# Performance work log

Measured on AMD Instinct MI355X. Metric: run time of the kernel, lower is better.

The kernel has to match this reference:

```python
import jax, jax.numpy as jnp
import numpy as np
import math

NUM_HEADS = 8

def setup_inputs() -> dict:
    key = jax.random.key(0)
    ks = jax.random.split(key, 20)
    N, n, M, E = 4096, 3, 16, 256
    nE = 65536
    s = lambda k, shape: (jax.random.normal(k, shape, jnp.float32) * 0.02)
    return {
        "equ": jax.random.normal(ks[0], (N, n, M), jnp.float32),
        "h": jax.random.normal(ks[1], (N, E), jnp.float32),
        "edge_index": jax.random.randint(ks[2], (2, nE), 0, N),
        "edge_fea": jax.random.normal(ks[3], (nE, 4), jnp.float32),
        "W_equ": s(ks[4], (M, E)),
        "W_gproj": s(ks[5], (E, 32)),
        "W_vg": s(ks[6], (E, E)),
        "W_g1": s(ks[7], (32 * 32, 2 * E)), "b_g1": jnp.zeros((2 * E,), jnp.float32),
        "W_g2": s(ks[8], (2 * E, E)), "b_g2": jnp.zeros((E,), jnp.float32),
        "W_q": s(ks[9], (2 * E, E)), "b_q": jnp.zeros((E,), jnp.float32),
        "W_k": s(ks[10], (2 * E, E)), "b_k": jnp.zeros((E,), jnp.float32),
        "W_v": s(ks[11], (2 * E, E)), "b_v": jnp.zeros((E,), jnp.float32),
        "W_ng": s(ks[12], (E, E)), "b_ng": jnp.zeros((E,), jnp.float32),
        "W_gout": s(ks[13], (E, E)),
        "W_gdec": s(ks[14], (E, M)),
        "W_hdec": s(ks[15], (E, E)), "b_hdec": jnp.zeros((E,), jnp.float32),
    }


def reference(equ, h, edge_index, edge_fea, W_equ, W_gproj, W_vg, W_g1, b_g1,
              W_g2, b_g2, W_q, b_q, W_k, b_k, W_v, b_v, W_ng, b_ng,
              W_gout, W_gdec, W_hdec, b_hdec):
    # edge_index / edge_fea are unused in the original forward (dead args).
    N, n, M = equ.shape
    E = W_equ.shape[1]
    H = NUM_HEADS
    D = E // H
    scaling = D ** -0.5
    sqrtE = math.sqrt(E)

    g_src = (equ @ W_equ) * sqrtE                     # [N, n, E]
    h_src = h * sqrtE                                 # [N, E]

    g2 = g_src @ W_gproj                              # [N, n, 32]
    gram = jnp.einsum('nia,nib->nab', g2, g2)         # [N, 32, 32]
    g2 = gram.reshape(N, 32 * 32)
    g2 = jax.nn.relu(g2 @ W_g1 + b_g1) @ W_g2 + b_g2  # [N, E]

    h2 = jnp.concatenate([g2, h_src], axis=-1)        # [N, 2E]
    q = ((h2 @ W_q + b_q) * scaling).reshape(N, H, D)
    k = (h2 @ W_k + b_k).reshape(N, H, D)
    v = (h2 @ W_v + b_v).reshape(N, H, D)
    vg = (g_src @ W_vg).reshape(N, n, H, D)           # [N, n, H, D]

    attn = jax.nn.softmax(jnp.einsum('nhd,mhd->hnm', q, k), axis=-1)  # [H, N, N]

    out_v = jnp.einsum('hnm,mhd->nhd', attn, v).reshape(N, E)
    h_src1 = out_v @ W_ng + b_ng                      # [N, E]

    # Same attention probs reused for the vector channel (torch does repeat+bmm;
    # we broadcast instead of materializing the repeated [n*H, N, N] tensor).
    out_g = jnp.einsum('hnm,mvhd->nvhd', attn, vg).reshape(N, n, E)
    g_src1 = out_g @ W_gout                           # [N, n, E]

    g_src = g_src + g_src1
    h_src = h_src + h_src1
    equ_out = g_src @ W_gdec                          # [N, n, M]
    h_out = h_src @ W_hdec + b_hdec                   # [N, E]
    return (equ_out, h_out)
```

## Files before the change

kernel.cpp:

```cpp
#include <hip/hip_runtime.h>
#include <hip/hip_bf16.h>

typedef __attribute__((ext_vector_type(8))) short short8;
typedef __attribute__((ext_vector_type(4))) float floatx4;

constexpr int N_ = 4096;
constexpr float SQRT_E = 16.0f;
constexpr float QSCALE = 0.17677669529663687f * 1.4426950408889634f;

__device__ __forceinline__ ushort f2bf(float x) {
  __hip_bfloat16 h = __float2bfloat16(x);
  return *reinterpret_cast<ushort*>(&h);
}
__device__ __forceinline__ float bf2f(ushort b) {
  unsigned int u = ((unsigned int)b) << 16;
  return __uint_as_float(u);
}

__device__ __forceinline__ float dpp_max16(float x) {
  int v = __float_as_int(x);
  int y;
  y = __builtin_amdgcn_update_dpp(v, v, 0x128, 0xf, 0xf, false);
  v = __float_as_int(fmaxf(__int_as_float(v), __int_as_float(y)));
  y = __builtin_amdgcn_update_dpp(v, v, 0x124, 0xf, 0xf, false);
  v = __float_as_int(fmaxf(__int_as_float(v), __int_as_float(y)));
  y = __builtin_amdgcn_update_dpp(v, v, 0x122, 0xf, 0xf, false);
  v = __float_as_int(fmaxf(__int_as_float(v), __int_as_float(y)));
  y = __builtin_amdgcn_update_dpp(v, v, 0x121, 0xf, 0xf, false);
  v = __float_as_int(fmaxf(__int_as_float(v), __int_as_float(y)));
  return __int_as_float(v);
}

__device__ __forceinline__ void do_transpose(
    const float* __restrict__ src, ushort* __restrict__ dsth,
    ushort* __restrict__ dstl, int R, int C, int lb, int cb_shift,
    float* smem, int hasLo)
{
  float (*tile)[33] = (float(*)[33])smem;
  const int r0 = (lb >> cb_shift) * 32;
  const int c0 = (lb & ((1 << cb_shift) - 1)) * 32;
  const int tx = threadIdx.x & 31, ty = threadIdx.x >> 5;
  #pragma unroll
  for (int p = 0; p < 4; ++p) {
    const int lr = p*8 + ty;
    tile[lr][tx] = (r0+lr < R && c0+tx < C) ? src[(size_t)(r0+lr)*C + c0 + tx] : 0.f;
  }
  __syncthreads();
  #pragma unroll
  for (int p = 0; p < 4; ++p) {
    const int dc = p*8 + ty;
    if (c0+dc < C && r0+tx < R) {
      const float v = tile[tx][dc];
      const ushort hi = f2bf(v);
      dsth[(size_t)(c0+dc)*R + r0 + tx] = hi;
      if (hasLo) dstl[(size_t)(c0+dc)*R + r0 + tx] = f2bf(v - bf2f(hi));
    }
  }
}

__global__ __launch_bounds__(256) void k_prep(
    const float* __restrict__ equ, const float* __restrict__ h,
    const float* __restrict__ W_equ, const float* __restrict__ W_gproj,
    const float* __restrict__ W_g1, const float* __restrict__ W_g2,
    const float* __restrict__ W_q, const float* __restrict__ W_k,
    const float* __restrict__ W_v, const float* __restrict__ W_vg,
    const float* __restrict__ W_ng, const float* __restrict__ W_gout,
    const float* __restrict__ W_hdec, const float* __restrict__ W_gdec,
    ushort* __restrict__ Wg1t, ushort* __restrict__ Wg2t,
    ushort* __restrict__ Wth, ushort* __restrict__ Wtl,
    ushort* __restrict__ Wvgt, ushort* __restrict__ Wngt,
    ushort* __restrict__ Wgoutt, ushort* __restrict__ Whdect,
    ushort* __restrict__ Wgdect,
    ushort* __restrict__ h2h, ushort* __restrict__ h2l,
    ushort* __restrict__ g_src_b, ushort* __restrict__ gram_b,
    float* __restrict__ pre0)
{
  __shared__ __align__(16) float smem[1120];
  const int b = blockIdx.x;
  const int t = threadIdx.x;

  if (b < 512) {
    do_transpose(W_g1, Wg1t, nullptr, 1024, 512, b, 4, smem, 0);
  } else if (b < 640) {
    do_transpose(W_g2, Wg2t, nullptr, 512, 256, b-512, 3, smem, 0);
  } else if (b < 768) {
    do_transpose(W_q, Wth, Wtl, 512, 256, b-640, 3, smem, 1);
  } else if (b < 896) {
    do_transpose(W_k, Wth + 256*512, Wtl + 256*512, 512, 256, b-768, 3, smem, 1);
  } else if (b < 1024) {
    do_transpose(W_v, Wth + 512*512, Wtl + 512*512, 512, 256, b-896, 3, smem, 1);
  } else if (b < 1088) {
    do_transpose(W_vg, Wvgt, nullptr, 256, 256, b-1024, 3, smem, 0);
  } else if (b < 1152) {
    do_transpose(W_ng, Wngt, nullptr, 256, 256, b-1088, 3, smem, 0);
  } else if (b < 1216) {
    do_transpose(W_gout, Wgoutt, nullptr, 256, 256, b-1152, 3, smem, 0);
  } else if (b < 1280) {
    do_transpose(W_hdec, Whdect, nullptr, 256, 256, b-1216, 3, smem, 0);
  } else if (b < 1288) {
    do_transpose(W_gdec, Wgdect, nullptr, 256, 16, b-1280, 0, smem, 0);
  } else if (b < 5384) {
    const int i = b - 1288;
    const float v = h[(size_t)i*256 + t] * SQRT_E;
    const ushort hi = f2bf(v);
    h2h[(size_t)i*512 + 256 + t] = hi;
    h2l[(size_t)i*512 + 256 + t] = f2bf(v - bf2f(hi));
  } else {
    float* eq   = smem;
    float* gs   = smem + 48;
    float* g2p  = smem + 816;
    float* part = smem + 912;
    const int i = b - 5384;
    if (t < 48) eq[t] = equ[(size_t)i*48 + t];
    __syncthreads();
    #pragma unroll
    for (int j = 0; j < 3; ++j) {
      float s = 0.f;
      #pragma unroll
      for (int m = 0; m < 16; ++m) s += eq[j*16+m] * W_equ[m*256 + t];
      s *= SQRT_E;
      gs[j*256 + t] = s;
      g_src_b[((size_t)i*3 + j)*256 + t] = f2bf(s);
    }
    __syncthreads();
    if (t < 192) {
      const int o = t % 96, half = t / 96;
      const int j = o >> 5, a = o & 31;
      const int e0 = half * 128;
      float s = 0.f;
      for (int e = 0; e < 128; ++e)
        s += gs[j*256 + e0 + e] * W_gproj[(size_t)(e0+e)*32 + a];
      part[t] = s;
    }
    __syncthreads();
    if (t < 96) g2p[t] = part[t] + part[96 + t];
    __syncthreads();
    #pragma unroll
    for (int r = 0; r < 4; ++r) {
      const int idx = r*256 + t;
      const int a = idx >> 5, bb = idx & 31;
      const float s = g2p[a]*g2p[bb] + g2p[32+a]*g2p[32+bb] + g2p[64+a]*g2p[64+bb];
      gram_b[(size_t)i*1024 + idx] = f2bf(s);
    }
    if (t < 192) {
      const int j = t >> 6, ks = (t >> 4) & 3, mc = t & 15;
      const int e0 = ks * 64;
      float s = 0.f;
      for (int e = 0; e < 64; ++e)
        s += gs[j*256 + e0 + e] * W_gdec[(size_t)(e0 + e)*16 + mc];
      part[t] = s;
    }
    __syncthreads();
    if (t < 48) {
      const int j = t >> 4, mc = t & 15;
      pre0[((size_t)i*3 + j)*16 + mc] =
          part[j*64 + mc] + part[j*64 + 16 + mc] +
          part[j*64 + 32 + mc] + part[j*64 + 48 + mc];
    }
  }
}

template<int KTOT>
__device__ __forceinline__ void gemm_core(
    const ushort* __restrict__ A, const ushort* __restrict__ Bt,
    int bM, int bN, floatx4 acc[4], ushort* As, ushort* Bs)
{
  const int t = threadIdx.x;
  const int wave = t >> 6, lane = t & 63, quad = lane >> 4, m = lane & 15;
  #pragma unroll
  for (int ct = 0; ct < 4; ++ct) acc[ct] = {0.f, 0.f, 0.f, 0.f};
  const int ca = t*2, cb = t*2 + 1;
  const int ra = ca >> 3, pa = ca & 7;
  const int rb = cb >> 3, pb = cb & 7;
  const ushort* pA0 = A  + (size_t)(bM+ra)*KTOT + pa*8;
  const ushort* pA1 = A  + (size_t)(bM+rb)*KTOT + pb*8;
  const ushort* pB0 = Bt + (size_t)(bN+ra)*KTOT + pa*8;
  const ushort* pB1 = Bt + (size_t)(bN+rb)*KTOT + pb*8;
  short8 rA0 = *(const short8*)pA0, rA1 = *(const short8*)pA1;
  short8 rB0 = *(const short8*)pB0, rB1 = *(const short8*)pB1;
  for (int k0 = 0; k0 < KTOT; k0 += 64) {
    __syncthreads();
    *(short8*)&As[ra*72 + pa*8] = rA0;
    *(short8*)&As[rb*72 + pb*8] = rA1;
    *(short8*)&Bs[ra*72 + pa*8] = rB0;
    *(short8*)&Bs[rb*72 + pb*8] = rB1;
    if (k0 + 64 < KTOT) {
      pA0 += 64; pA1 += 64; pB0 += 64; pB1 += 64;
      rA0 = *(const short8*)pA0; rA1 = *(const short8*)pA1;
      rB0 = *(const short8*)pB0; rB1 = *(const short8*)pB1;
    }
    __syncthreads();
    #pragma unroll
    for (int ks = 0; ks < 2; ++ks) {
      const short8 af = *(const short8*)&As[(wave*16 + m)*72 + ks*32 + quad*8];
      #pragma unroll
      for (int ct = 0; ct < 4; ++ct) {
        const short8 bf = *(const short8*)&Bs[(ct*16 + m)*72 + ks*32 + quad*8];
        acc[ct] = __builtin_amdgcn_mfma_f32_16x16x32_bf16(af, bf, acc[ct], 0, 0, 0);
      }
    }
  }
}

template<int KTOT>
__device__ __forceinline__ void gemm_core3(
    const ushort* __restrict__ Ah, const ushort* __restrict__ Al,
    const ushort* __restrict__ Bth, const ushort* __restrict__ Btl,
    int bM, int bN, floatx4 acc[4],
    ushort* Ash, ushort* Asl, ushort* Bsh, ushort* Bsl)
{
  const int t = threadIdx.x;
  const int wave = t >> 6, lane = t & 63, quad = lane >> 4, m = lane & 15;
  #pragma unroll
  for (int ct = 0; ct < 4; ++ct) acc[ct] = {0.f, 0.f, 0.f, 0.f};
  const int ca = t*2, cb = t*2 + 1;
  const int ra = ca >> 3, pa = ca & 7;
  const int rb = cb >> 3, pb = cb & 7;
  const ushort* pAh0 = Ah  + (size_t)(bM+ra)*KTOT + pa*8;
  const ushort* pAh1 = Ah  + (size_t)(bM+rb)*KTOT + pb*8;
  const ushort* pAl0 = Al  + (size_t)(bM+ra)*KTOT + pa*8;
  const ushort* pAl1 = Al  + (size_t)(bM+rb)*KTOT + pb*8;
  const ushort* pBh0 = Bth + (size_t)(bN+ra)*KTOT + pa*8;
  const ushort* pBh1 = Bth + (size_t)(bN+rb)*KTOT + pb*8;
  const ushort* pBl0 = Btl + (size_t)(bN+ra)*KTOT + pa*8;
  const ushort* pBl1 = Btl + (size_t)(bN+rb)*KTOT + pb*8;
  short8 rAh0 = *(const short8*)pAh0, rAh1 = *(const short8*)pAh1;
  short8 rAl0 = *(const short8*)pAl0, rAl1 = *(const short8*)pAl1;
  short8 rBh0 = *(const short8*)pBh0, rBh1 = *(const short8*)pBh1;
  short8 rBl0 = *(const short8*)pBl0, rBl1 = *(const short8*)pBl1;
  for (int k0 = 0; k0 < KTOT; k0 += 64) {
    __syncthreads();
    *(short8*)&Ash[ra*72 + pa*8] = rAh0;
    *(short8*)&Ash[rb*72 + pb*8] = rAh1;
    *(short8*)&Asl[ra*72 + pa*8] = rAl0;
    *(short8*)&Asl[rb*72 + pb*8] = rAl1;
    *(short8*)&Bsh[ra*72 + pa*8] = rBh0;
    *(short8*)&Bsh[rb*72 + pb*8] = rBh1;
    *(short8*)&Bsl[ra*72 + pa*8] = rBl0;
    *(short8*)&Bsl[rb*72 + pb*8] = rBl1;
    if (k0 + 64 < KTOT) {
      pAh0 += 64; pAh1 += 64; pAl0 += 64; pAl1 += 64;
      pBh0 += 64; pBh1 += 64; pBl0 += 64; pBl1 += 64;
      rAh0 = *(const short8*)pAh0; rAh1 = *(const short8*)pAh1;
      rAl0 = *(const short8*)pAl0; rAl1 = *(const short8*)pAl1;
      rBh0 = *(const short8*)pBh0; rBh1 = *(const short8*)pBh1;
      rBl0 = *(const short8*)pBl0; rBl1 = *(const short8*)pBl1;
    }
    __syncthreads();
    #pragma unroll
    for (int ks = 0; ks < 2; ++ks) {
      const short8 ah = *(const short8*)&Ash[(wave*16 + m)*72 + ks*32 + quad*8];
      const short8 al = *(const short8*)&Asl[(wave*16 + m)*72 + ks*32 + quad*8];
      #pragma unroll
      for (int ct = 0; ct < 4; ++ct) {
        const short8 bh = *(const short8*)&Bsh[(ct*16 + m)*72 + ks*32 + quad*8];
        const short8 bl = *(const short8*)&Bsl[(ct*16 + m)*72 + ks*32 + quad*8];
        acc[ct] = __builtin_amdgcn_mfma_f32_16x16x32_bf16(ah, bl, acc[ct], 0, 0, 0);
        acc[ct] = __builtin_amdgcn_mfma_f32_16x16x32_bf16(al, bh, acc[ct], 0, 0, 0);
        acc[ct] = __builtin_amdgcn_mfma_f32_16x16x32_bf16(ah, bh, acc[ct], 0, 0, 0);
      }
    }
  }
}

__global__ __launch_bounds__(256) void k_g1(
    const ushort* __restrict__ gram_b, const ushort* __restrict__ Wg1t,
    const float* __restrict__ b_g1, ushort* __restrict__ hidden)
{
  __shared__ __align__(16) ushort As[64*72], Bs[64*72];
  floatx4 acc[4];
  const int bM = blockIdx.x*64, bN = blockIdx.y*64;
  gemm_core<1024>(gram_b, Wg1t, bM, bN, acc, As, Bs);
  const int lane = threadIdx.x & 63, wave = threadIdx.x >> 6;
  const int quad = lane >> 4, m = lane & 15;
  #pragma unroll
  for (int ct = 0; ct < 4; ++ct) {
    const int c = bN + ct*16 + m;
    #pragma unroll
    for (int r = 0; r < 4; ++r) {
      const int i = bM + wave*16 + quad*4 + r;
      hidden[(size_t)i*512 + c] = f2bf(fmaxf(acc[ct][r] + b_g1[c], 0.f));
    }
  }
}

__global__ __launch_bounds__(256) void k_g2(
    const ushort* __restrict__ hidden, const ushort* __restrict__ Wg2t,
    const float* __restrict__ b_g2, ushort* __restrict__ h2h, ushort* __restrict__ h2l)
{
  __shared__ __align__(16) ushort As[64*72], Bs[64*72];
  floatx4 acc[4];
  const int bM = blockIdx.x*64, bN = blockIdx.y*64;
  gemm_core<512>(hidden, Wg2t, bM, bN, acc, As, Bs);
  const int lane = threadIdx.x & 63, wave = threadIdx.x >> 6;
  const int quad = lane >> 4, m = lane & 15;
  #pragma unroll
  for (int ct = 0; ct < 4; ++ct) {
    const int c = bN + ct*16 + m;
    #pragma unroll
    for (int r = 0; r < 4; ++r) {
      const int i = bM + wave*16 + quad*4 + r;
      const float s = acc[ct][r] + b_g2[c];
      const ushort hi = f2bf(s);
      h2h[(size_t)i*512 + c] = hi;
      h2l[(size_t)i*512 + c] = f2bf(s - bf2f(hi));
    }
  }
}

__global__ __launch_bounds__(256) void k_g34(
    const ushort* __restrict__ h2h, const ushort* __restrict__ h2l,
    const ushort* __restrict__ Wth, const ushort* __restrict__ Wtl,
    const float* __restrict__ b_q, const float* __restrict__ b_k,
    const float* __restrict__ b_v,
    const ushort* __restrict__ g_src_b, const ushort* __restrict__ Wvgt,
    float* __restrict__ q_ws, ushort* __restrict__ kh,
    ushort* __restrict__ vt)
{
  __shared__ __align__(16) ushort S0[64*72], S1[64*72], S2[64*72], S3[64*72];
  const int lb = blockIdx.y*192 + blockIdx.x;
  const int lane = threadIdx.x & 63, wave = threadIdx.x >> 6;
  const int quad = lane >> 4, m = lane & 15;
  floatx4 acc[4];
  if (lb < 768) {
    const int bM = (lb & 63)*64, bN = (lb >> 6)*64;
    if (bN < 512) {
      gemm_core3<512>(h2h, h2l, Wth, Wtl, bM, bN, acc, S0, S1, S2, S3);
      #pragma unroll
      for (int ct = 0; ct < 4; ++ct) {
        const int c = bN + ct*16 + m;
        #pragma unroll
        for (int r = 0; r < 4; ++r) {
          const int i = bM + wave*16 + quad*4 + r;
          if (c < 256) {
            const float s = acc[ct][r] + b_q[c];
            q_ws[((size_t)(c >> 5)*N_ + i)*32 + (c & 31)] = s * QSCALE;
          } else {
            const int cc = c - 256;
            const float s = acc[ct][r] + b_k[cc];
            kh[((size_t)(cc >> 5)*N_ + i)*32 + (cc & 31)] = f2bf(s);
          }
        }
      }
    } else {
      gemm_core<512>(h2h, Wth, bM, bN, acc, S0, S1);
      #pragma unroll
      for (int ct = 0; ct < 4; ++ct) {
        const int cc = bN + ct*16 + m - 512;
        #pragma unroll
        for (int r = 0; r < 4; ++r) {
          const int i = bM + wave*16 + quad*4 + r;
          const float s = acc[ct][r] + b_v[cc];
          vt[((size_t)(cc >> 5)*128 + (cc & 31))*N_ + i] = f2bf(s);
        }
      }
    }
  } else {
    const int lb2 = lb - 768;
    const int bM = (lb2 >> 2)*64, bN = (lb2 & 3)*64;
    gemm_core<256>(g_src_b, Wvgt, bM, bN, acc, S0, S1);
    #pragma unroll
    for (int ct = 0; ct < 4; ++ct) {
      const int c = bN + ct*16 + m;
      const int hh = c >> 5, d = c & 31;
      #pragma unroll
      for (int r = 0; r < 4; ++r) {
        const int i3 = bM + wave*16 + quad*4 + r;
        const int i = i3 / 3, j = i3 - 3*i;
        vt[((size_t)hh*128 + 32 + j*32 + d)*N_ + i] = f2bf(acc[ct][r]);
      }
    }
  }
}

__global__ __launch_bounds__(256, 4) void k3_attn(
    const float* __restrict__ q_ws, const ushort* __restrict__ kh,
    const ushort* __restrict__ vt,
    ushort* __restrict__ Po0, ushort* __restrict__ Po1,
    ushort* __restrict__ Po2, ushort* __restrict__ Po3,
    float* __restrict__ Pml)
{
  __shared__ __align__(16) ushort Khs[64*40];
  __shared__ __align__(16) ushort Vs[128*64];
  __shared__ __align__(16) ushort Pl[4*16*72];
  __shared__ float li_s[64];

  const int t    = threadIdx.x;
  const int wave = t >> 6;
  const int lane = t & 63;
  const int quad = lane >> 4;
  const int m    = lane & 15;
  const int h    = blockIdx.y;
  const int s    = blockIdx.z;
  const int n0q  = blockIdx.x * 64;

  const int ktb = s * 16;
  const int kte = ktb + 16;

  union { short8 v; ushort u[8]; } Aqh, Aql;
  {
    const float* qp = q_ws + ((size_t)h*N_ + n0q + wave*16 + m)*32 + quad*8;
    #pragma unroll
    for (int jj = 0; jj < 8; ++jj) {
      const float x = qp[jj];
      const ushort hi = f2bf(x);
      Aqh.u[jj] = hi;
      Aql.u[jj] = f2bf(x - bf2f(hi));
    }
  }

  union { short8 v; ushort u[8]; } onesf;
  {
    const ushort ov = (m == 0) ? (ushort)0x3F80 : (ushort)0;
    #pragma unroll
    for (int jj = 0; jj < 8; ++jj) onesf.u[jj] = ov;
  }

  floatx4 Of[9];
  #pragma unroll
  for (int nt = 0; nt < 9; ++nt) Of[nt] = {0.f, 0.f, 0.f, 0.f};
  float mi[4];
  #pragma unroll
  for (int r = 0; r < 4; ++r) mi[r] = -3.0e38f;

  const int krow = t >> 2, kch = (t & 3) * 8;

  const ushort* pKh = kh + ((size_t)h*N_ + ktb*64 + krow)*32 + kch;
  const ushort* pV[4];
  int wV[4];
  #pragma unroll
  for (int p = 0; p < 4; ++p) {
    const int idx = p*256 + t, row = idx >> 3, g = idx & 7;
    pV[p] = vt + ((size_t)h*128 + row)*N_ + ktb*64 + g*8;
    wV[p] = (row*8 + (g ^ (row & 7)))*8;
  }

  short8 rK0 = *(const short8*)pKh;
  short8 rV[4];
  #pragma unroll
  for (int p = 0; p < 4; ++p) rV[p] = *(const short8*)pV[p];

  for (int kt = ktb; kt < kte; ++kt) {
    __syncthreads();
    *(short8*)&Khs[krow*40 + kch] = rK0;
    #pragma unroll
    for (int p = 0; p < 4; ++p) *(short8*)&Vs[wV[p]] = rV[p];
    if (kt + 1 < kte) {
      pKh += 2048;
      rK0 = *(const short8*)pKh;
      #pragma unroll
      for (int p = 0; p < 4; ++p) { pV[p] += 64; rV[p] = *(const short8*)pV[p]; }
    }
    __syncthreads();

    floatx4 sf[4];
    #pragma unroll
    for (int kb = 0; kb < 4; ++kb) {
      const short8 bkh = *(const short8*)&Khs[(kb*16 + m)*40 + quad*8];
      floatx4 sv = {0.f, 0.f, 0.f, 0.f};
      sv = __builtin_amdgcn_mfma_f32_16x16x32_bf16(Aql.v, bkh, sv, 0, 0, 0);
      sv = __builtin_amdgcn_mfma_f32_16x16x32_bf16(Aqh.v, bkh, sv, 0, 0, 0);
      sf[kb] = sv;
    }

    float tm[4];
    bool need = false;
    #pragma unroll
    for (int r = 0; r < 4; ++r) {
      float nm = fmaxf(fmaxf(sf[0][r], sf[1][r]), fmaxf(sf[2][r], sf[3][r]));
      tm[r] = dpp_max16(nm);
      need |= (tm[r] > mi[r] + 20.f);
    }
    if (__any(need)) {
      #pragma unroll
      for (int r = 0; r < 4; ++r) {
        const float mn = fmaxf(mi[r], tm[r]);
        const float al = exp2f(mi[r] - mn);
        mi[r] = mn;
        #pragma unroll
        for (int nt = 0; nt < 9; ++nt) Of[nt][r] *= al;
      }
    }
    float base[4];
    #pragma unroll
    for (int r = 0; r < 4; ++r) base[r] = 1064866805.0f - mi[r]*8388608.0f;
    #pragma unroll
    for (int kb = 0; kb < 4; ++kb)
      #pragma unroll
      for (int r = 0; r < 4; ++r) {
        int pi = (int)(sf[kb][r]*8388608.0f + base[r]);
        pi = pi < 0 ? 0 : pi;
        Pl[wave*1152 + (quad*4 + r)*72 + kb*16 + m] = (ushort)(pi >> 16);
      }

    #pragma unroll
    for (int ks = 0; ks < 2; ++ks) {
      const short8 ap = *(const short8*)&Pl[wave*1152 + m*72 + ks*32 + quad*8];
      #pragma unroll
      for (int nt = 0; nt < 8; ++nt) {
        const int row = nt*16 + m;
        const int pos = (ks*4 + quad) ^ (row & 7);
        const short8 bv = *(const short8*)&Vs[(row*8 + pos)*8];
        Of[nt] = __builtin_amdgcn_mfma_f32_16x16x32_bf16(ap, bv, Of[nt], 0, 0, 0);
      }
      Of[8] = __builtin_amdgcn_mfma_f32_16x16x32_bf16(ap, onesf.v, Of[8], 0, 0, 0);
    }
  }

  if (m == 0) {
    #pragma unroll
    for (int r = 0; r < 4; ++r) li_s[wave*16 + quad*4 + r] = Of[8][r];
  }
  __syncthreads();
  const floatx4 liv = *(const floatx4*)&li_s[wave*16 + quad*4];
  float linv[4];
  #pragma unroll
  for (int r = 0; r < 4; ++r) linv[r] = 1.0f / liv[r];

  ushort* Po = (s == 0) ? Po0 : ((s == 1) ? Po1 : ((s == 2) ? Po2 : Po3));
  #pragma unroll
  for (int nt = 0; nt < 8; ++nt) {
    #pragma unroll
    for (int r = 0; r < 4; ++r) {
      const int n = n0q + wave*16 + quad*4 + r;
      Po[((size_t)h*N_ + n)*128 + nt*16 + m] = f2bf(Of[nt][r] * linv[r]);
    }
  }
  if (m == 0) {
    #pragma unroll
    for (int r = 0; r < 4; ++r) {
      const int n = n0q + wave*16 + quad*4 + r;
      Pml[(((size_t)s*8 + h)*N_ + n)*2 + 0] = mi[r];
      Pml[(((size_t)s*8 + h)*N_ + n)*2 + 1] = Of[8][r];
    }
  }
}

__global__ __launch_bounds__(256) void k_merge(
    const ushort* __restrict__ Po0, const ushort* __restrict__ Po1,
    const ushort* __restrict__ Po2, const ushort* __restrict__ Po3,
    const float* __restrict__ Pml,
    ushort* __restrict__ out_v_b, ushort* __restrict__ out_g_b)
{
  const int idx = blockIdx.x*256 + threadIdx.x;
  const int c0 = (idx & 15) * 8;
  const int n  = (idx >> 4) & 4095;
  const int h  = idx >> 16;
  float mm[4], ll[4];
  #pragma unroll
  for (int s = 0; s < 4; ++s) {
    mm[s] = Pml[(((size_t)s*8 + h)*N_ + n)*2 + 0];
    ll[s] = Pml[(((size_t)s*8 + h)*N_ + n)*2 + 1];
  }
  const float M = fmaxf(fmaxf(mm[0], mm[1]), fmaxf(mm[2], mm[3]));
  float w[4], tot = 0.f;
  #pragma unroll
  for (int s = 0; s < 4; ++s) { w[s] = exp2f(mm[s] - M) * ll[s]; tot += w[s]; }
  const float inv = 1.0f / tot;
  union { short8 v; ushort u[8]; } a, b, c, d, res;
  a.v = *(const short8*)&Po0[((size_t)h*N_ + n)*128 + c0];
  b.v = *(const short8*)&Po1[((size_t)h*N_ + n)*128 + c0];
  c.v = *(const short8*)&Po2[((size_t)h*N_ + n)*128 + c0];
  d.v = *(const short8*)&Po3[((size_t)h*N_ + n)*128 + c0];
  #pragma unroll
  for (int j = 0; j < 8; ++j)
    res.u[j] = f2bf((w[0]*bf2f(a.u[j]) + w[1]*bf2f(b.u[j]) +
                     w[2]*bf2f(c.u[j]) + w[3]*bf2f(d.u[j])) * inv);
  if (c0 < 32) {
    *(short8*)&out_v_b[(size_t)n*256 + h*32 + c0] = res.v;
  } else {
    const int j = (c0 - 32) >> 5, cc = (c0 - 32) & 31;
    *(short8*)&out_g_b[((size_t)n*3 + j)*256 + h*32 + cc] = res.v;
  }
}

__global__ __launch_bounds__(256) void k56ab(
    const ushort* __restrict__ out_v_b, const ushort* __restrict__ Wngt,
    const float* __restrict__ b_ng, const float* __restrict__ h,
    ushort* __restrict__ tmp_b,
    const ushort* __restrict__ out_g_b, const ushort* __restrict__ Wgoutt,
    ushort* __restrict__ gsum_b)
{
  __shared__ __align__(16) ushort As[64*72], Bs[64*72];
  floatx4 acc[4];
  const int lane = threadIdx.x & 63, wave = threadIdx.x >> 6;
  const int quad = lane >> 4, m = lane & 15;
  const int bN = blockIdx.y*64;
  if (blockIdx.x < 64) {
    const int bM = blockIdx.x*64;
    gemm_core<256>(out_v_b, Wngt, bM, bN, acc, As, Bs);
    #pragma unroll
    for (int ct = 0; ct < 4; ++ct) {
      const int c = bN + ct*16 + m;
      #pragma unroll
      for (int r = 0; r < 4; ++r) {
        const int i = bM + wave*16 + quad*4 + r;
        tmp_b[(size_t)i*256 + c] =
            f2bf(acc[ct][r] + b_ng[c] + h[(size_t)i*256 + c] * SQRT_E);
      }
    }
  } else {
    const int bM = (blockIdx.x - 64)*64;
    gemm_core<256>(out_g_b, Wgoutt, bM, bN, acc, As, Bs);
    #pragma unroll
    for (int ct = 0; ct < 4; ++ct) {
      const int c = bN + ct*16 + m;
      #pragma unroll
      for (int r = 0; r < 4; ++r) {
        const int i = bM + wave*16 + quad*4 + r;
        gsum_b[(size_t)i*256 + c] = f2bf(acc[ct][r]);
      }
    }
  }
}

__global__ __launch_bounds__(256) void k56cd(
    const ushort* __restrict__ tmp_b, const ushort* __restrict__ Whdect,
    const float* __restrict__ b_hdec,
    const ushort* __restrict__ gsum_b, const ushort* __restrict__ Wgdect,
    const float* __restrict__ pre0,
    float* __restrict__ out)
{
  __shared__ __align__(16) ushort As[64*72], Bs[64*72];
  const int t = threadIdx.x;
  const int lane = t & 63, wave = t >> 6;
  const int quad = lane >> 4, m = lane & 15;
  if (blockIdx.x < 64) {
    floatx4 acc[4];
    const int bM = blockIdx.x*64, bN = blockIdx.y*64;
    gemm_core<256>(tmp_b, Whdect, bM, bN, acc, As, Bs);
    #pragma unroll
    for (int ct = 0; ct < 4; ++ct) {
      const int c = bN + ct*16 + m;
      #pragma unroll
      for (int r = 0; r < 4; ++r) {
        const int i = bM + wave*16 + quad*4 + r;
        out[196608 + (size_t)i*256 + c] = acc[ct][r] + b_hdec[c];
      }
    }
  } else if (blockIdx.y == 0) {
    const int bM = (blockIdx.x - 64)*64;
    floatx4 acc = {0.f, 0.f, 0.f, 0.f};
    const int row = t >> 2, kq = (t & 3) * 8;
    for (int k0 = 0; k0 < 256; k0 += 32) {
      __syncthreads();
      *(short8*)&As[row*40 + kq] = *(const short8*)&gsum_b[(size_t)(bM+row)*256 + k0 + kq];
      if (t < 64)
        *(short8*)&Bs[(t>>2)*40 + kq] = *(const short8*)&Wgdect[(size_t)(t>>2)*256 + k0 + kq];
      __syncthreads();
      const short8 af = *(const short8*)&As[(wave*16 + m)*40 + quad*8];
      const short8 bf = *(const short8*)&Bs[m*40 + quad*8];
      acc = __builtin_amdgcn_mfma_f32_16x16x32_bf16(af, bf, acc, 0, 0, 0);
    }
    #pragma unroll
    for (int r = 0; r < 4; ++r) {
      const int i3 = bM + wave*16 + quad*4 + r;
      out[(size_t)i3*16 + m] = acc[r] + pre0[(size_t)i3*16 + m];
    }
  }
}

extern "C" void kernel_launch(void* const* d_in, const int* in_sizes, int n_in,
                              void* d_out, int out_size, void* d_ws, size_t ws_size,
                              hipStream_t stream) {
  const float* equ    = (const float*)d_in[0];
  const float* h      = (const float*)d_in[1];
  const float* W_equ  = (const float*)d_in[4];
  const float* W_gproj= (const float*)d_in[5];
  const float* W_vg   = (const float*)d_in[6];
  const float* W_g1   = (const float*)d_in[7];
  const float* b_g1   = (const float*)d_in[8];
  const float* W_g2   = (const float*)d_in[9];
  const float* b_g2   = (const float*)d_in[10];
  const float* W_q    = (const float*)d_in[11];
  const float* b_q    = (const float*)d_in[12];
  const float* W_k    = (const float*)d_in[13];
  const float* b_k    = (const float*)d_in[14];
  const float* W_v    = (const float*)d_in[15];
  const float* b_v    = (const float*)d_in[16];
  const float* W_ng   = (const float*)d_in[17];
  const float* b_ng   = (const float*)d_in[18];
  const float* W_gout = (const float*)d_in[19];
  const float* W_gdec = (const float*)d_in[20];
  const float* W_hdec = (const float*)d_in[21];
  const float* b_hdec = (const float*)d_in[22];
  float* out = (float*)d_out;

  char* wsb = (char*)d_ws;
  constexpr size_t MiB = 1048576;
  float*  q_ws    = (float*) (wsb +  0*MiB);
  ushort* kh      = (ushort*)(wsb +  4*MiB);
  float*  Pml     = (float*) (wsb +  6*MiB);
  float*  pre0    = (float*) (wsb +  7*MiB);
  ushort* vt      = (ushort*)(wsb +  8*MiB);
  ushort* h2h     = (ushort*)(wsb + 17*MiB);
  ushort* h2l     = (ushort*)(wsb + 21*MiB);
  ushort* g_src_b = (ushort*)(wsb + 25*MiB);
  ushort* wbase   = (ushort*)(wsb + 31*MiB);
  ushort* Wg1t = wbase;
  ushort* Wg2t = wbase + 524288;
  ushort* Wth  = wbase + 655360;
  ushort* Wtl  = wbase + 1048576;
  ushort* Wvgt = wbase + 1441792;
  ushort* gram_b  = (ushort*)(wsb + 34*MiB);
  ushort* hidden  = (ushort*)(wsb + 42*MiB);
  ushort* Po0     = (ushort*)(wsb + 17*MiB);
  ushort* Po1     = (ushort*)(wsb + 25*MiB);
  ushort* Po2     = (ushort*)(wsb + 34*MiB);
  ushort* Po3     = (ushort*)(wsb + 42*MiB);
  ushort* wbase2  = (ushort*)(wsb + 50*MiB);
  ushort* Wngt   = wbase2;
  ushort* Wgoutt = wbase2 + 65536;
  ushort* Whdect = wbase2 + 131072;
  ushort* Wgdect = wbase2 + 196608;
  ushort* out_v_b = (ushort*)(wsb +  4*MiB);
  ushort* out_g_b = (ushort*)(wsb +  8*MiB);
  ushort* tmp_b   = (ushort*)(wsb + 17*MiB);
  ushort* gsum_b  = (ushort*)(wsb + 25*MiB);

  k_prep<<<9480, 256, 0, stream>>>(
      equ, h, W_equ, W_gproj, W_g1, W_g2, W_q, W_k, W_v,
      W_vg, W_ng, W_gout, W_hdec, W_gdec,
      Wg1t, Wg2t, Wth, Wtl, Wvgt, Wngt, Wgoutt, Whdect, Wgdect,
      h2h, h2l, g_src_b, gram_b, pre0);

  k_g1<<<dim3(64, 8), 256, 0, stream>>>(gram_b, Wg1t, b_g1, hidden);
  k_g2<<<dim3(64, 4), 256, 0, stream>>>(hidden, Wg2t, b_g2, h2h, h2l);
  k_g34<<<dim3(192, 8), 256, 0, stream>>>(h2h, h2l, Wth, Wtl, b_q, b_k, b_v,
                                          g_src_b, Wvgt, q_ws, kh, vt);

  dim3 g3(64, 8, 4);
  k3_attn<<<g3, 256, 0, stream>>>(q_ws, kh, vt, Po0, Po1, Po2, Po3, Pml);
  k_merge<<<2048, 256, 0, stream>>>(Po0, Po1, Po2, Po3, Pml, out_v_b, out_g_b);

  k56ab<<<dim3(256, 4), 256, 0, stream>>>(out_v_b, Wngt, b_ng, h, tmp_b,
                                          out_g_b, Wgoutt, gsum_b);
  k56cd<<<dim3(256, 4), 256, 0, stream>>>(tmp_b, Whdect, b_hdec,
                                          gsum_b, Wgdect, pre0, out);
}
```

Baseline: 278.2 us.

## Transpose attention MFMA to keep P in registers and use three KV splits

```diff
diff --git a/kernel.cpp b/kernel.cpp
--- a/kernel.cpp
+++ b/kernel.cpp
@@ -2,6 +2,7 @@
 #include <hip/hip_bf16.h>
 
 typedef __attribute__((ext_vector_type(8))) short short8;
+typedef __attribute__((ext_vector_type(4))) short bhalf4;
 typedef __attribute__((ext_vector_type(4))) float floatx4;
 
 constexpr int N_ = 4096;
@@ -15,20 +16,6 @@
 __device__ __forceinline__ float bf2f(ushort b) {
   unsigned int u = ((unsigned int)b) << 16;
   return __uint_as_float(u);
-}
-
-__device__ __forceinline__ float dpp_max16(float x) {
-  int v = __float_as_int(x);
-  int y;
-  y = __builtin_amdgcn_update_dpp(v, v, 0x128, 0xf, 0xf, false);
-  v = __float_as_int(fmaxf(__int_as_float(v), __int_as_float(y)));
-  y = __builtin_amdgcn_update_dpp(v, v, 0x124, 0xf, 0xf, false);
-  v = __float_as_int(fmaxf(__int_as_float(v), __int_as_float(y)));
-  y = __builtin_amdgcn_update_dpp(v, v, 0x122, 0xf, 0xf, false);
-  v = __float_as_int(fmaxf(__int_as_float(v), __int_as_float(y)));
-  y = __builtin_amdgcn_update_dpp(v, v, 0x121, 0xf, 0xf, false);
-  v = __float_as_int(fmaxf(__int_as_float(v), __int_as_float(y)));
-  return __int_as_float(v);
 }
 
 __device__ __forceinline__ void do_transpose(
@@ -373,16 +360,14 @@
   }
 }
 
-__global__ __launch_bounds__(256, 4) void k3_attn(
+__global__ __launch_bounds__(256, 6) void k3_attn(
     const float* __restrict__ q_ws, const ushort* __restrict__ kh,
     const ushort* __restrict__ vt,
-    ushort* __restrict__ Po0, ushort* __restrict__ Po1,
-    ushort* __restrict__ Po2, ushort* __restrict__ Po3,
+    ushort* __restrict__ Po0, ushort* __restrict__ Po1, ushort* __restrict__ Po2,
     float* __restrict__ Pml)
 {
   __shared__ __align__(16) ushort Khs[64*40];
   __shared__ __align__(16) ushort Vs[128*64];
-  __shared__ __align__(16) ushort Pl[4*16*72];
   __shared__ float li_s[64];
 
   const int t    = threadIdx.x;
@@ -394,8 +379,8 @@
   const int s    = blockIdx.z;
   const int n0q  = blockIdx.x * 64;
 
-  const int ktb = s * 16;
-  const int kte = ktb + 16;
+  const int ktb = (s == 0) ? 0  : (s == 1 ? 22 : 43);
+  const int kte = (s == 0) ? 22 : (s == 1 ? 43 : 64);
 
   union { short8 v; ushort u[8]; } Aqh, Aql;
   {
@@ -416,23 +401,25 @@
     for (int jj = 0; jj < 8; ++jj) onesf.u[jj] = ov;
   }
 
-  floatx4 Of[9];
-  #pragma unroll
-  for (int nt = 0; nt < 9; ++nt) Of[nt] = {0.f, 0.f, 0.f, 0.f};
-  float mi[4];
-  #pragma unroll
-  for (int r = 0; r < 4; ++r) mi[r] = -3.0e38f;
+  floatx4 Of[8];
+  #pragma unroll
+  for (int nt = 0; nt < 8; ++nt) Of[nt] = {0.f, 0.f, 0.f, 0.f};
+  floatx4 Of8 = {0.f, 0.f, 0.f, 0.f};
+  float mi = -3.0e38f;
 
   const int krow = t >> 2, kch = (t & 3) * 8;
-
   const ushort* pKh = kh + ((size_t)h*N_ + ktb*64 + krow)*32 + kch;
+
   const ushort* pV[4];
-  int wV[4];
+  int wv0[4], wv1[4];
   #pragma unroll
   for (int p = 0; p < 4; ++p) {
     const int idx = p*256 + t, row = idx >> 3, g = idx & 7;
     pV[p] = vt + ((size_t)h*128 + row)*N_ + ktb*64 + g*8;
-    wV[p] = (row*8 + (g ^ (row & 7)))*8;
+    const int sb0  = 32*(g>>2) + 16*(g&1) + 4*((g>>1)&1);
+    const int blk0 = sb0 >> 3, off = sb0 & 4, r7 = row & 7;
+    wv0[p] = row*64 + ((blk0       ^ r7) * 8) + off;
+    wv1[p] = row*64 + (((blk0 + 1) ^ r7) * 8) + off;
   }
 
   short8 rK0 = *(const short8*)pKh;
@@ -440,11 +427,18 @@
   #pragma unroll
   for (int p = 0; p < 4; ++p) rV[p] = *(const short8*)pV[p];
 
+  const int x7 = m & 7;
+
   for (int kt = ktb; kt < kte; ++kt) {
     __syncthreads();
     *(short8*)&Khs[krow*40 + kch] = rK0;
     #pragma unroll
-    for (int p = 0; p < 4; ++p) *(short8*)&Vs[wV[p]] = rV[p];
+    for (int p = 0; p < 4; ++p) {
+      union { short8 v; bhalf4 h2[2]; } tmp;
+      tmp.v = rV[p];
+      *(bhalf4*)&Vs[wv0[p]] = tmp.h2[0];
+      *(bhalf4*)&Vs[wv1[p]] = tmp.h2[1];
+    }
     if (kt + 1 < kte) {
       pKh += 2048;
       rK0 = *(const short8*)pKh;
@@ -458,114 +452,98 @@
     for (int kb = 0; kb < 4; ++kb) {
       const short8 bkh = *(const short8*)&Khs[(kb*16 + m)*40 + quad*8];
       floatx4 sv = {0.f, 0.f, 0.f, 0.f};
-      sv = __builtin_amdgcn_mfma_f32_16x16x32_bf16(Aql.v, bkh, sv, 0, 0, 0);
-      sv = __builtin_amdgcn_mfma_f32_16x16x32_bf16(Aqh.v, bkh, sv, 0, 0, 0);
+      sv = __builtin_amdgcn_mfma_f32_16x16x32_bf16(bkh, Aql.v, sv, 0, 0, 0);
+      sv = __builtin_amdgcn_mfma_f32_16x16x32_bf16(bkh, Aqh.v, sv, 0, 0, 0);
       sf[kb] = sv;
     }
 
-    float tm[4];
-    bool need = false;
-    #pragma unroll
-    for (int r = 0; r < 4; ++r) {
-      float nm = fmaxf(fmaxf(sf[0][r], sf[1][r]), fmaxf(sf[2][r], sf[3][r]));
-      tm[r] = dpp_max16(nm);
-      need |= (tm[r] > mi[r] + 20.f);
-    }
-    if (__any(need)) {
-      #pragma unroll
-      for (int r = 0; r < 4; ++r) {
-        const float mn = fmaxf(mi[r], tm[r]);
-        const float al = exp2f(mi[r] - mn);
-        mi[r] = mn;
-        #pragma unroll
-        for (int nt = 0; nt < 9; ++nt) Of[nt][r] *= al;
-      }
-    }
-    float base[4];
-    #pragma unroll
-    for (int r = 0; r < 4; ++r) base[r] = 1064866805.0f - mi[r]*8388608.0f;
-    #pragma unroll
-    for (int kb = 0; kb < 4; ++kb)
-      #pragma unroll
-      for (int r = 0; r < 4; ++r) {
-        int pi = (int)(sf[kb][r]*8388608.0f + base[r]);
-        pi = pi < 0 ? 0 : pi;
-        Pl[wave*1152 + (quad*4 + r)*72 + kb*16 + m] = (ushort)(pi >> 16);
-      }
+    float nm = fmaxf(fmaxf(sf[0][0], sf[0][1]), fmaxf(sf[0][2], sf[0][3]));
+    nm = fmaxf(nm, fmaxf(fmaxf(sf[1][0], sf[1][1]), fmaxf(sf[1][2], sf[1][3])));
+    nm = fmaxf(nm, fmaxf(fmaxf(sf[2][0], sf[2][1]), fmaxf(sf[2][2], sf[2][3])));
+    nm = fmaxf(nm, fmaxf(fmaxf(sf[3][0], sf[3][1]), fmaxf(sf[3][2], sf[3][3])));
+    nm = fmaxf(nm, __shfl_xor(nm, 16));
+    nm = fmaxf(nm, __shfl_xor(nm, 32));
+
+    if (__any(nm > mi + 20.f)) {
+      const float mn = fmaxf(mi, nm);
+      const float al = exp2f(mi - mn);
+      mi = mn;
+      #pragma unroll
+      for (int nt = 0; nt < 8; ++nt) {
+        Of[nt][0] *= al; Of[nt][1] *= al; Of[nt][2] *= al; Of[nt][3] *= al;
+      }
+      Of8[0] *= al; Of8[1] *= al; Of8[2] *= al; Of8[3] *= al;
+    }
+
+    const float base = 1064866805.0f - mi*8388608.0f;
+    union { short8 v; unsigned int u[4]; } pk[2];
+    #pragma unroll
+    for (int kb = 0; kb < 4; ++kb) {
+      int p0 = (int)(sf[kb][0]*8388608.0f + base); p0 = p0 < 0 ? 0 : p0;
+      int p1 = (int)(sf[kb][1]*8388608.0f + base); p1 = p1 < 0 ? 0 : p1;
+      int p2 = (int)(sf[kb][2]*8388608.0f + base); p2 = p2 < 0 ? 0 : p2;
+      int p3 = (int)(sf[kb][3]*8388608.0f + base); p3 = p3 < 0 ? 0 : p3;
+      pk[kb >> 1].u[(kb & 1)*2 + 0] = ((unsigned)p0 >> 16) | ((unsigned)p1 & 0xffff0000u);
+      pk[kb >> 1].u[(kb & 1)*2 + 1] = ((unsigned)p2 >> 16) | ((unsigned)p3 & 0xffff0000u);
+    }
 
     #pragma unroll
     for (int ks = 0; ks < 2; ++ks) {
-      const short8 ap = *(const short8*)&Pl[wave*1152 + m*72 + ks*32 + quad*8];
       #pragma unroll
       for (int nt = 0; nt < 8; ++nt) {
-        const int row = nt*16 + m;
-        const int pos = (ks*4 + quad) ^ (row & 7);
-        const short8 bv = *(const short8*)&Vs[(row*8 + pos)*8];
-        Of[nt] = __builtin_amdgcn_mfma_f32_16x16x32_bf16(ap, bv, Of[nt], 0, 0, 0);
-      }
-      Of[8] = __builtin_amdgcn_mfma_f32_16x16x32_bf16(ap, onesf.v, Of[8], 0, 0, 0);
-    }
-  }
-
-  if (m == 0) {
-    #pragma unroll
-    for (int r = 0; r < 4; ++r) li_s[wave*16 + quad*4 + r] = Of[8][r];
-  }
+        const short8 av = *(const short8*)&Vs[(nt*16 + m)*64 + (((ks*4 + quad) ^ x7) * 8)];
+        Of[nt] = __builtin_amdgcn_mfma_f32_16x16x32_bf16(av, pk[ks].v, Of[nt], 0, 0, 0);
+      }
+      Of8 = __builtin_amdgcn_mfma_f32_16x16x32_bf16(onesf.v, pk[ks].v, Of8, 0, 0, 0);
+    }
+  }
+
+  if (quad == 0) li_s[wave*16 + m] = Of8[0];
   __syncthreads();
-  const floatx4 liv = *(const floatx4*)&li_s[wave*16 + quad*4];
-  float linv[4];
-  #pragma unroll
-  for (int r = 0; r < 4; ++r) linv[r] = 1.0f / liv[r];
-
-  ushort* Po = (s == 0) ? Po0 : ((s == 1) ? Po1 : ((s == 2) ? Po2 : Po3));
+  const float linv = 1.0f / li_s[wave*16 + m];
+
+  ushort* Po = (s == 0) ? Po0 : ((s == 1) ? Po1 : Po2);
+  const int n = n0q + wave*16 + m;
   #pragma unroll
   for (int nt = 0; nt < 8; ++nt) {
-    #pragma unroll
-    for (int r = 0; r < 4; ++r) {
-      const int n = n0q + wave*16 + quad*4 + r;
-      Po[((size_t)h*N_ + n)*128 + nt*16 + m] = f2bf(Of[nt][r] * linv[r]);
-    }
-  }
-  if (m == 0) {
-    #pragma unroll
-    for (int r = 0; r < 4; ++r) {
-      const int n = n0q + wave*16 + quad*4 + r;
-      Pml[(((size_t)s*8 + h)*N_ + n)*2 + 0] = mi[r];
-      Pml[(((size_t)s*8 + h)*N_ + n)*2 + 1] = Of[8][r];
-    }
+    unsigned int lo = (unsigned)f2bf(Of[nt][0] * linv) | ((unsigned)f2bf(Of[nt][1] * linv) << 16);
+    unsigned int hi = (unsigned)f2bf(Of[nt][2] * linv) | ((unsigned)f2bf(Of[nt][3] * linv) << 16);
+    uint2 pkd; pkd.x = lo; pkd.y = hi;
+    *(uint2*)&Po[((size_t)h*N_ + n)*128 + nt*16 + quad*4] = pkd;
+  }
+  if (quad == 0) {
+    Pml[(((size_t)s*8 + h)*N_ + n)*2 + 0] = mi;
+    Pml[(((size_t)s*8 + h)*N_ + n)*2 + 1] = Of8[0];
   }
 }
 
 __global__ __launch_bounds__(256) void k_merge(
     const ushort* __restrict__ Po0, const ushort* __restrict__ Po1,
-    const ushort* __restrict__ Po2, const ushort* __restrict__ Po3,
-    const float* __restrict__ Pml,
+    const ushort* __restrict__ Po2, const float* __restrict__ Pml,
     ushort* __restrict__ out_v_b, ushort* __restrict__ out_g_b)
 {
   const int idx = blockIdx.x*256 + threadIdx.x;
   const int c0 = (idx & 15) * 8;
   const int n  = (idx >> 4) & 4095;
   const int h  = idx >> 16;
-  float mm[4], ll[4];
-  #pragma unroll
-  for (int s = 0; s < 4; ++s) {
-    mm[s] = Pml[(((size_t)s*8 + h)*N_ + n)*2 + 0];
-    ll[s] = Pml[(((size_t)s*8 + h)*N_ + n)*2 + 1];
-  }
-  const float M = fmaxf(fmaxf(mm[0], mm[1]), fmaxf(mm[2], mm[3]));
-  float w[4], tot = 0.f;
-  #pragma unroll
-  for (int s = 0; s < 4; ++s) { w[s] = exp2f(mm[s] - M) * ll[s]; tot += w[s]; }
-  const float inv = 1.0f / tot;
-  union { short8 v; ushort u[8]; } a, b, c, d, res;
+  const float m1 = Pml[(((size_t)0*8 + h)*N_ + n)*2 + 0];
+  const float l1 = Pml[(((size_t)0*8 + h)*N_ + n)*2 + 1];
+  const float m2 = Pml[(((size_t)1*8 + h)*N_ + n)*2 + 0];
+  const float l2 = Pml[(((size_t)1*8 + h)*N_ + n)*2 + 1];
+  const float m3 = Pml[(((size_t)2*8 + h)*N_ + n)*2 + 0];
+  const float l3 = Pml[(((size_t)2*8 + h)*N_ + n)*2 + 1];
+  const float M = fmaxf(fmaxf(m1, m2), m3);
+  const float w1 = exp2f(m1 - M) * l1;
+  const float w2 = exp2f(m2 - M) * l2;
+  const float w3 = exp2f(m3 - M) * l3;
+  const float inv = 1.0f / (w1 + w2 + w3);
+  union { short8 v; ushort u[8]; } a, b, c, res;
   a.v = *(const short8*)&Po0[((size_t)h*N_ + n)*128 + c0];
   b.v = *(const short8*)&Po1[((size_t)h*N_ + n)*128 + c0];
   c.v = *(const short8*)&Po2[((size_t)h*N_ + n)*128 + c0];
-  d.v = *(const short8*)&Po3[((size_t)h*N_ + n)*128 + c0];
   #pragma unroll
   for (int j = 0; j < 8; ++j)
-    res.u[j] = f2bf((w[0]*bf2f(a.u[j]) + w[1]*bf2f(b.u[j]) +
-                     w[2]*bf2f(c.u[j]) + w[3]*bf2f(d.u[j])) * inv);
+    res.u[j] = f2bf((w1*bf2f(a.u[j]) + w2*bf2f(b.u[j]) + w3*bf2f(c.u[j])) * inv);
   if (c0 < 32) {
     *(short8*)&out_v_b[(size_t)n*256 + h*32 + c0] = res.v;
   } else {
@@ -707,7 +685,6 @@
   ushort* Po0     = (ushort*)(wsb + 17*MiB);
   ushort* Po1     = (ushort*)(wsb + 25*MiB);
   ushort* Po2     = (ushort*)(wsb + 34*MiB);
-  ushort* Po3     = (ushort*)(wsb + 42*MiB);
   ushort* wbase2  = (ushort*)(wsb + 50*MiB);
   ushort* Wngt   = wbase2;
   ushort* Wgoutt = wbase2 + 65536;
@@ -729,9 +706,9 @@
   k_g34<<<dim3(192, 8), 256, 0, stream>>>(h2h, h2l, Wth, Wtl, b_q, b_k, b_v,
                                           g_src_b, Wvgt, q_ws, kh, vt);
 
-  dim3 g3(64, 8, 4);
-  k3_attn<<<g3, 256, 0, stream>>>(q_ws, kh, vt, Po0, Po1, Po2, Po3, Pml);
-  k_merge<<<2048, 256, 0, stream>>>(Po0, Po1, Po2, Po3, Pml, out_v_b, out_g_b);
+  dim3 g3(64, 8, 3);
+  k3_attn<<<g3, 256, 0, stream>>>(q_ws, kh, vt, Po0, Po1, Po2, Pml);
+  k_merge<<<2048, 256, 0, stream>>>(Po0, Po1, Po2, Pml, out_v_b, out_g_b);
 
   k56ab<<<dim3(256, 4), 256, 0, stream>>>(out_v_b, Wngt, b_ng, h, tmp_b,
                                           out_g_b, Wgoutt, gsum_b);
```

Measured after the change: 471.2 us. +69.4%, slower.
